# Optimization experiments

Measured on AMD Instinct MI355X. Metric: run time of the kernel, lower is better.

Reference implementation:

```python
import jax, jax.numpy as jnp
import numpy as np

EMBED_DIM = 512
NUM_HEADS = 8
HEAD_DIM = EMBED_DIM // NUM_HEADS
SCALE = HEAD_DIM ** -0.5
B, N = 4, 2048


def setup_inputs() -> dict:
    key = jax.random.key(0)
    ks = jax.random.split(key, 6)
    x = jax.random.normal(ks[0], (B, N, EMBED_DIM), dtype=jnp.float32)
    mask = jnp.ones((B, N, N), dtype=jnp.int32)
    # nn.Linear params: weight [out, in], bias [out]
    lim_qkv = 1.0 / np.sqrt(EMBED_DIM)
    qkv_w = jax.random.uniform(ks[1], (3 * EMBED_DIM, EMBED_DIM), jnp.float32, -lim_qkv, lim_qkv)
    qkv_b = jax.random.uniform(ks[2], (3 * EMBED_DIM,), jnp.float32, -lim_qkv, lim_qkv)
    proj_w = jax.random.uniform(ks[3], (EMBED_DIM, EMBED_DIM), jnp.float32, -lim_qkv, lim_qkv)
    proj_b = jax.random.uniform(ks[4], (EMBED_DIM,), jnp.float32, -lim_qkv, lim_qkv)
    return {"x": x, "qkv_w": qkv_w, "qkv_b": qkv_b, "proj_w": proj_w, "proj_b": proj_b, "mask": mask}


def reference(x, qkv_w, qkv_b, proj_w, proj_b, mask):
    Bb, Nn, C = x.shape
    qkv = (jnp.einsum('bnc,oc->bno', x, qkv_w) + qkv_b).reshape(Bb, Nn, 3, NUM_HEADS, HEAD_DIM)
    qkv = jnp.transpose(qkv, (2, 0, 3, 1, 4))
    q, k, v = qkv[0], qkv[1], qkv[2]
    # full score matrix [B,H,N,N] (faithful to the unfused original)
    attn = jnp.einsum('bhnd,bhmd->bhnm', q, k) * SCALE
    attn = jnp.where(mask[:, None, :, :] == 0, -jnp.inf, attn)
    attn = jax.nn.softmax(attn, axis=-1)
    out = jnp.einsum('bhnm,bhmd->bhnd', attn, v)
    out = jnp.transpose(out, (0, 2, 1, 3)).reshape(Bb, Nn, C)
    out = jnp.einsum('bnc,oc->bno', out, proj_w) + proj_b
    return out
```

## Files before the change

kernel.cpp:

```cpp
#include <hip/hip_runtime.h>
#include <hip/hip_bf16.h>
#include <stdint.h>

#define NB 4
#define NH 8
#define SEQ 2048
#define HD 64
#define CDIM 512

using bf16 = __hip_bfloat16;
typedef __attribute__((ext_vector_type(8))) short short8;
typedef __attribute__((ext_vector_type(4))) short short4_t;
typedef __attribute__((ext_vector_type(4))) float f32x4;

#define NEG_BIG (-3.0e38f)
#define SOFT_C 0.18033688011112042f

__device__ __forceinline__ short bf16_bits(float x) {
  return __builtin_bit_cast(short, __float2bfloat16(x));
}

__device__ __forceinline__ void gld_lds16(const void* g, void* l) {
  __builtin_amdgcn_global_load_lds(
      (const __attribute__((address_space(1))) unsigned int*)g,
      (__attribute__((address_space(3))) unsigned int*)l, 16, 0, 0);
}

#define X4 1048576
#define Q4 196608
#define P4 65536
__global__ __launch_bounds__(256) void prep_cvt(const float* __restrict__ x,
                                                const float* __restrict__ wq,
                                                const float* __restrict__ wp,
                                                short* __restrict__ xb,
                                                short* __restrict__ wqb,
                                                short* __restrict__ wpb) {
  int idx = blockIdx.x * 256 + threadIdx.x;
  int stride = gridDim.x * 256;
  for (int i = idx; i < X4 + Q4 + P4; i += stride) {
    const float* src; short* dst; int off;
    if (i < X4)            { src = x;  dst = xb;  off = i; }
    else if (i < X4 + Q4)  { src = wq; dst = wqb; off = i - X4; }
    else                   { src = wp; dst = wpb; off = i - X4 - Q4; }
    f32x4 v = *(const f32x4*)(src + (size_t)off * 4);
    short4_t o;
    o[0] = bf16_bits(v[0]); o[1] = bf16_bits(v[1]);
    o[2] = bf16_bits(v[2]); o[3] = bf16_bits(v[3]);
    *(short4_t*)(dst + (size_t)off * 4) = o;
  }
}

__global__ __launch_bounds__(256) void qkv_union(const short* __restrict__ Xb,
                                                 const short* __restrict__ Wb,
                                                 const float* __restrict__ bias,
                                                 const int* __restrict__ mask,
                                                 unsigned long long* __restrict__ bits,
                                                 bf16* __restrict__ q,
                                                 bf16* __restrict__ k,
                                                 bf16* __restrict__ vt) {
  __shared__ short Alds[128][32];
  __shared__ short Blds[128][32];
  const int tid = threadIdx.x;
  const int lane = tid & 63;
  const int w = tid >> 6;

  if (blockIdx.x < 512) {
    int wave_g = blockIdx.x * 4 + w;
#pragma unroll 1
    for (int i = 0; i < 32; i++) {
      size_t c = (size_t)i * 2048 + wave_g;
      size_t base = c * 256;
      int v0 = mask[base + 0 * 64 + lane];
      int v1 = mask[base + 1 * 64 + lane];
      int v2 = mask[base + 2 * 64 + lane];
      int v3 = mask[base + 3 * 64 + lane];
      unsigned long long w0 = __ballot(v0 != 0);
      unsigned long long w1 = __ballot(v1 != 0);
      unsigned long long w2 = __ballot(v2 != 0);
      unsigned long long w3 = __ballot(v3 != 0);
      if (lane == 0) {
        bits[c * 4 + 0] = w0; bits[c * 4 + 1] = w1;
        bits[c * 4 + 2] = w2; bits[c * 4 + 3] = w3;
      }
    }
    return;
  }

  const int g = blockIdx.x - 512;
  const int wm = w >> 1, wn = w & 1;
  const int row0 = (g & 63) * 128;
  const int col0 = (g >> 6) * 128;
  const bool isv = (col0 >= 1024);

  f32x4 acc[4][4] = {};
  const int cl = lane & 15;
  const int quad = lane >> 4;

  const int st_r = lane >> 2;
  const int st_gc = (lane & 3) ^ (st_r & 3);
  const int st_col = st_gc * 8;
  const int fc = (quad ^ (cl & 3)) * 8;

  for (int kk = 0; kk < 512; kk += 32) {
#pragma unroll
    for (int t = 0; t < 2; t++) {
      int R = w * 32 + t * 16;
      gld_lds16(&Xb[(size_t)(row0 + R + st_r) * 512 + kk + st_col], &Alds[R][0]);
      gld_lds16(&Wb[(size_t)(col0 + R + st_r) * 512 + kk + st_col], &Blds[R][0]);
    }
    __syncthreads();
    short8 a[4], b[4];
#pragma unroll
    for (int i = 0; i < 4; i++) a[i] = *(const short8*)&Alds[wm * 64 + i * 16 + cl][fc];
#pragma unroll
    for (int j = 0; j < 4; j++) b[j] = *(const short8*)&Blds[wn * 64 + j * 16 + cl][fc];
    if (!isv) {
#pragma unroll
      for (int i = 0; i < 4; i++)
#pragma unroll
        for (int j = 0; j < 4; j++)
          acc[i][j] = __builtin_amdgcn_mfma_f32_16x16x32_bf16(a[i], b[j], acc[i][j], 0, 0, 0);
    } else {
#pragma unroll
      for (int i = 0; i < 4; i++)
#pragma unroll
        for (int j = 0; j < 4; j++)
          acc[i][j] = __builtin_amdgcn_mfma_f32_16x16x32_bf16(b[j], a[i], acc[i][j], 0, 0, 0);
    }
    __syncthreads();
  }

  if (!isv) {
#pragma unroll
    for (int i = 0; i < 4; i++) {
#pragma unroll
      for (int j = 0; j < 4; j++) {
        int col = col0 + wn * 64 + j * 16 + cl;
        float bv = bias[col];
        int which = col >> 9;
        int c = col & 511;
        int h = c >> 6, d = c & 63;
#pragma unroll
        for (int r = 0; r < 4; r++) {
          int row = row0 + wm * 64 + i * 16 + quad * 4 + r;
          int bb = row >> 11, n = row & 2047;
          float val = acc[i][j][r] + bv;
          size_t bh = (size_t)bb * NH + h;
          if (which == 0)      q[(bh * SEQ + n) * HD + d] = __float2bfloat16(val * SOFT_C);
          else                 k[(bh * SEQ + n) * HD + d] = __float2bfloat16(val);
        }
      }
    }
  } else {
#pragma unroll
    for (int i = 0; i < 4; i++) {
#pragma unroll
      for (int j = 0; j < 4; j++) {
        int nrow = row0 + wm * 64 + i * 16 + cl;
        int bb = nrow >> 11, n = nrow & 2047;
#pragma unroll
        for (int r = 0; r < 4; r++) {
          int col = col0 + wn * 64 + j * 16 + quad * 4 + r;
          float bv = bias[col];
          int c = col & 511;
          int h = c >> 6, d = c & 63;
          float val = acc[i][j][r] + bv;
          size_t bh = (size_t)bb * NH + h;
          vt[(bh * HD + d) * SEQ + n] = __float2bfloat16(val);
        }
      }
    }
  }
}

__global__ __launch_bounds__(256) void flash_attn(const bf16* __restrict__ qg,
                                                  const bf16* __restrict__ kg,
                                                  const bf16* __restrict__ vg,
                                                  const unsigned long long* __restrict__ mbits,
                                                  bf16* __restrict__ attn_out) {
  __shared__ short Klds[2][64][64];
  __shared__ short Vlds[2][64][64];
  __shared__ short Plds[4][2][16][72];
  __shared__ unsigned long long Mlds[2][128];

  const int tid = threadIdx.x;
  const int lane = tid & 63;
  const int w = tid >> 6;
  const int qt = blockIdx.x;
  const int h = blockIdx.y;
  const int b = blockIdx.z;

  const size_t bh = (size_t)b * NH + h;
  const bf16* qp = qg + bh * SEQ * HD;
  const bf16* kp = kg + bh * SEQ * HD;
  const bf16* vp = vg + bh * HD * SEQ;

  const int cl = lane & 15;
  const int quad = lane >> 4;
  const int koff = quad * 8;
  const int qrow_w = qt * 128 + w * 32;

  const int c0 = ((quad ^ (cl & 7)) * 8);

  const int st_row = lane >> 3;
  const int st_chunk = (lane & 7) ^ st_row;
  const int st_col = st_chunk * 8;

  short8 aq[2][2];
#pragma unroll
  for (int g = 0; g < 2; g++) {
    aq[g][0] = *(const short8*)&qp[(size_t)(qrow_w + g * 16 + cl) * HD + koff];
    aq[g][1] = *(const short8*)&qp[(size_t)(qrow_w + g * 16 + cl) * HD + 32 + koff];
  }

  f32x4 o[2][4] = {};
  float l_l[2] = {0.f, 0.f};

#pragma unroll
  for (int t = 0; t < 2; t++) {
    int rbase = w * 16 + t * 8;
    gld_lds16(&kp[(size_t)(rbase + st_row) * HD + st_col], &Klds[0][rbase][0]);
    gld_lds16(&vp[(size_t)(rbase + st_row) * SEQ + st_col], &Vlds[0][rbase][0]);
  }
  if (tid < 128) Mlds[0][tid] = mbits[((size_t)b * SEQ + qt * 128 + tid) * (SEQ / 64) + 0];

  for (int kt = 0; kt < 32; kt++) {
    const int cur = kt & 1;
    __syncthreads();

    if (kt + 1 < 32) {
      const int kb2 = (kt + 1) * 64;
#pragma unroll
      for (int t = 0; t < 2; t++) {
        int rbase = w * 16 + t * 8;
        gld_lds16(&kp[(size_t)(kb2 + rbase + st_row) * HD + st_col], &Klds[cur ^ 1][rbase][0]);
        gld_lds16(&vp[(size_t)(rbase + st_row) * SEQ + kb2 + st_col], &Vlds[cur ^ 1][rbase][0]);
      }
      if (tid < 128)
        Mlds[cur ^ 1][tid] = mbits[((size_t)b * SEQ + qt * 128 + tid) * (SEQ / 64) + kt + 1];
    }

    short8 k0[4], k1[4], vb[2][4];
#pragma unroll
    for (int nb = 0; nb < 4; nb++) {
      k0[nb] = *(const short8*)&Klds[cur][nb * 16 + cl][c0];
      k1[nb] = *(const short8*)&Klds[cur][nb * 16 + cl][c0 ^ 32];
    }
#pragma unroll
    for (int ks = 0; ks < 2; ks++)
#pragma unroll
      for (int db = 0; db < 4; db++)
        vb[ks][db] = *(const short8*)&Vlds[cur][db * 16 + cl][c0 ^ (ks * 32)];

    f32x4 s[2][4];
#pragma unroll
    for (int g = 0; g < 2; g++)
#pragma unroll
      for (int nb = 0; nb < 4; nb++) {
        f32x4 z = {0.f, 0.f, 0.f, 0.f};
        z = __builtin_amdgcn_mfma_f32_16x16x32_bf16(k0[nb], aq[g][0], z, 0, 0, 0);
        s[g][nb] = __builtin_amdgcn_mfma_f32_16x16x32_bf16(k1[nb], aq[g][1], z, 0, 0, 0);
      }

#pragma unroll
    for (int g = 0; g < 2; g++) {
      unsigned long long wd = Mlds[cur][w * 32 + g * 16 + cl];
      if (wd != ~0ULL) {
#pragma unroll
        for (int nb = 0; nb < 4; nb++)
#pragma unroll
          for (int r = 0; r < 4; r++)
            if (!((wd >> (nb * 16 + quad * 4 + r)) & 1ULL)) s[g][nb][r] = NEG_BIG;
      }
      float ps = 0.f;
#pragma unroll
      for (int nb = 0; nb < 4; nb++)
#pragma unroll
        for (int r = 0; r < 4; r++) {
          float p = __builtin_amdgcn_exp2f(s[g][nb][r]);
          s[g][nb][r] = p;
          ps += p;
        }
      ps += __shfl_xor(ps, 16);
      ps += __shfl_xor(ps, 32);
      l_l[g] += ps;
#pragma unroll
      for (int nb = 0; nb < 4; nb++) {
        short4_t pk;
        pk[0] = bf16_bits(s[g][nb][0]); pk[1] = bf16_bits(s[g][nb][1]);
        pk[2] = bf16_bits(s[g][nb][2]); pk[3] = bf16_bits(s[g][nb][3]);
        *(short4_t*)&Plds[w][g][cl][nb * 16 + quad * 4] = pk;
      }
    }

#pragma unroll
    for (int g = 0; g < 2; g++)
#pragma unroll
      for (int ks = 0; ks < 2; ks++) {
        short8 pa = *(const short8*)&Plds[w][g][cl][ks * 32 + koff];
#pragma unroll
        for (int db = 0; db < 4; db++)
          o[g][db] = __builtin_amdgcn_mfma_f32_16x16x32_bf16(pa, vb[ks][db], o[g][db], 0, 0, 0);
      }
  }

#pragma unroll
  for (int g = 0; g < 2; g++) {
    float inv = 1.0f / l_l[g];
#pragma unroll
    for (int r = 0; r < 4; r++) {
      float ir = __shfl(inv, (lane & 48) + quad * 4 + r);
      int row = qrow_w + g * 16 + quad * 4 + r;
#pragma unroll
      for (int db = 0; db < 4; db++) {
        float val = o[g][db][r] * ir;
        attn_out[((size_t)b * SEQ + row) * CDIM + h * 64 + db * 16 + cl] = __float2bfloat16(val);
      }
    }
  }
}

__global__ __launch_bounds__(256) void proj_gemm(const bf16* __restrict__ X,
                                                 const short* __restrict__ Wb,
                                                 const float* __restrict__ bias,
                                                 float* __restrict__ out) {
  __shared__ short Alds[128][32];
  __shared__ short Blds[128][32];
  const int tid = threadIdx.x;
  const int lane = tid & 63;
  const int w = tid >> 6;
  const int wm = w >> 1, wn = w & 1;
  const int row0 = blockIdx.x * 128;
  const int col0 = blockIdx.y * 128;

  f32x4 acc[4][4] = {};
  const int cl = lane & 15;
  const int quad = lane >> 4;

  const int st_r = lane >> 2;
  const int st_gc = (lane & 3) ^ (st_r & 3);
  const int st_col = st_gc * 8;
  const int fc = (quad ^ (cl & 3)) * 8;

  for (int kk = 0; kk < 512; kk += 32) {
#pragma unroll
    for (int t = 0; t < 2; t++) {
      int R = w * 32 + t * 16;
      gld_lds16(&X[(size_t)(row0 + R + st_r) * 512 + kk + st_col], &Alds[R][0]);
      gld_lds16(&Wb[(size_t)(col0 + R + st_r) * 512 + kk + st_col], &Blds[R][0]);
    }
    __syncthreads();
    short8 a[4], b[4];
#pragma unroll
    for (int i = 0; i < 4; i++) a[i] = *(const short8*)&Alds[wm * 64 + i * 16 + cl][fc];
#pragma unroll
    for (int j = 0; j < 4; j++) b[j] = *(const short8*)&Blds[wn * 64 + j * 16 + cl][fc];
#pragma unroll
    for (int i = 0; i < 4; i++)
#pragma unroll
      for (int j = 0; j < 4; j++)
        acc[i][j] = __builtin_amdgcn_mfma_f32_16x16x32_bf16(a[i], b[j], acc[i][j], 0, 0, 0);
    __syncthreads();
  }

#pragma unroll
  for (int i = 0; i < 4; i++) {
#pragma unroll
    for (int j = 0; j < 4; j++) {
      int col = col0 + wn * 64 + j * 16 + cl;
      float bv = bias[col];
#pragma unroll
      for (int r = 0; r < 4; r++) {
        int row = row0 + wm * 64 + i * 16 + quad * 4 + r;
        out[(size_t)row * 512 + col] = acc[i][j][r] + bv;
      }
    }
  }
}

extern "C" void kernel_launch(void* const* d_in, const int* in_sizes, int n_in,
                              void* d_out, int out_size, void* d_ws, size_t ws_size,
                              hipStream_t stream) {
  const float* x      = (const float*)d_in[0];
  const float* qkv_w  = (const float*)d_in[1];
  const float* qkv_b  = (const float*)d_in[2];
  const float* proj_w = (const float*)d_in[3];
  const float* proj_b = (const float*)d_in[4];
  const int*   mask   = (const int*)d_in[5];
  float* out = (float*)d_out;

  char* ws = (char*)d_ws;
  bf16* q    = (bf16*)(ws);
  bf16* k    = (bf16*)(ws + 8388608);
  bf16* vt   = (bf16*)(ws + 16777216);
  bf16* attn = (bf16*)(ws + 25165824);
  short* xb  = (short*)(ws + 25165824);
  unsigned long long* mbits = (unsigned long long*)(ws + 33554432);
  short* wqb = (short*)(ws + 35651584);
  short* wpb = (short*)(ws + 37224448);

  prep_cvt<<<dim3(1280), 256, 0, stream>>>(x, qkv_w, proj_w, xb, wqb, wpb);
  qkv_union<<<dim3(512 + 768), 256, 0, stream>>>(xb, wqb, qkv_b, mask, mbits, q, k, vt);
  flash_attn<<<dim3(SEQ / 128, NH, NB), 256, 0, stream>>>(q, k, vt, mbits, attn);
  proj_gemm<<<dim3(64, 4), 256, 0, stream>>>(attn, wpb, proj_b, out);
}
```

Measured before the change: 225.5 us.

## Compute softmax row sums via MFMA with ones, load mask bits into registers

The softmax denominator is now accumulated by an extra MFMA of the bf16 P tile against a ones vector, replacing per-lane sums and cross-lane shuffles. Mask words are prefetched straight from global memory into registers, so the shared-memory mask buffer goes away. K/V fragment reads move ahead of the next-tile prefetch, the barrier moves to the end of the loop, and bf16 packing uses two 32-bit words. This trims VALU and shuffle work but adds MFMA issue per tile, and the row sum now uses bf16-rounded probabilities.

```diff
diff --git a/kernel.cpp b/kernel.cpp
--- a/kernel.cpp
+++ b/kernel.cpp
@@ -11,6 +11,7 @@
 using bf16 = __hip_bfloat16;
 typedef __attribute__((ext_vector_type(8))) short short8;
 typedef __attribute__((ext_vector_type(4))) short short4_t;
+typedef __attribute__((ext_vector_type(2))) unsigned int uint2_t;
 typedef __attribute__((ext_vector_type(4))) float f32x4;
 
 #define NEG_BIG (-3.0e38f)
@@ -18,6 +19,17 @@
 
 __device__ __forceinline__ short bf16_bits(float x) {
   return __builtin_bit_cast(short, __float2bfloat16(x));
+}
+
+__device__ __forceinline__ void pack_p4(float a, float b, float c, float d, short* dst) {
+  unsigned lo = (unsigned)(unsigned short)bf16_bits(a) |
+                ((unsigned)(unsigned short)bf16_bits(b) << 16);
+  unsigned hi = (unsigned)(unsigned short)bf16_bits(c) |
+                ((unsigned)(unsigned short)bf16_bits(d) << 16);
+  uint2_t t;
+  t[0] = lo;
+  t[1] = hi;
+  *(uint2_t*)dst = t;
 }
 
 __device__ __forceinline__ void gld_lds16(const void* g, void* l) {
@@ -181,7 +193,6 @@
   __shared__ short Klds[2][64][64];
   __shared__ short Vlds[2][64][64];
   __shared__ short Plds[4][2][16][72];
-  __shared__ unsigned long long Mlds[2][128];
 
   const int tid = threadIdx.x;
   const int lane = tid & 63;
@@ -206,6 +217,9 @@
   const int st_chunk = (lane & 7) ^ st_row;
   const int st_col = st_chunk * 8;
 
+  const unsigned long long* mr0 = mbits + ((size_t)b * SEQ + qt * 128 + w * 32 + cl) * 32;
+  const unsigned long long* mr1 = mr0 + 16 * 32;
+
   short8 aq[2][2];
 #pragma unroll
   for (int g = 0; g < 2; g++) {
@@ -213,8 +227,12 @@
     aq[g][1] = *(const short8*)&qp[(size_t)(qrow_w + g * 16 + cl) * HD + 32 + koff];
   }
 
+  short8 ones;
+#pragma unroll
+  for (int i = 0; i < 8; i++) ones[i] = (short)0x3F80;
+
   f32x4 o[2][4] = {};
-  float l_l[2] = {0.f, 0.f};
+  f32x4 ol[2] = {};
 
 #pragma unroll
   for (int t = 0; t < 2; t++) {
@@ -222,11 +240,25 @@
     gld_lds16(&kp[(size_t)(rbase + st_row) * HD + st_col], &Klds[0][rbase][0]);
     gld_lds16(&vp[(size_t)(rbase + st_row) * SEQ + st_col], &Vlds[0][rbase][0]);
   }
-  if (tid < 128) Mlds[0][tid] = mbits[((size_t)b * SEQ + qt * 128 + tid) * (SEQ / 64) + 0];
+  unsigned long long wd_next[2];
+  wd_next[0] = mr0[0];
+  wd_next[1] = mr1[0];
+  __syncthreads();
 
   for (int kt = 0; kt < 32; kt++) {
     const int cur = kt & 1;
-    __syncthreads();
+
+    short8 k0[4], k1[4], vb[2][4];
+#pragma unroll
+    for (int nb = 0; nb < 4; nb++) {
+      k0[nb] = *(const short8*)&Klds[cur][nb * 16 + cl][c0];
+      k1[nb] = *(const short8*)&Klds[cur][nb * 16 + cl][c0 ^ 32];
+    }
+#pragma unroll
+    for (int ks = 0; ks < 2; ks++)
+#pragma unroll
+      for (int db = 0; db < 4; db++)
+        vb[ks][db] = *(const short8*)&Vlds[cur][db * 16 + cl][c0 ^ (ks * 32)];
 
     if (kt + 1 < 32) {
       const int kb2 = (kt + 1) * 64;
@@ -236,21 +268,12 @@
         gld_lds16(&kp[(size_t)(kb2 + rbase + st_row) * HD + st_col], &Klds[cur ^ 1][rbase][0]);
         gld_lds16(&vp[(size_t)(rbase + st_row) * SEQ + kb2 + st_col], &Vlds[cur ^ 1][rbase][0]);
       }
-      if (tid < 128)
-        Mlds[cur ^ 1][tid] = mbits[((size_t)b * SEQ + qt * 128 + tid) * (SEQ / 64) + kt + 1];
-    }
-
-    short8 k0[4], k1[4], vb[2][4];
-#pragma unroll
-    for (int nb = 0; nb < 4; nb++) {
-      k0[nb] = *(const short8*)&Klds[cur][nb * 16 + cl][c0];
-      k1[nb] = *(const short8*)&Klds[cur][nb * 16 + cl][c0 ^ 32];
-    }
-#pragma unroll
-    for (int ks = 0; ks < 2; ks++)
-#pragma unroll
-      for (int db = 0; db < 4; db++)
-        vb[ks][db] = *(const short8*)&Vlds[cur][db * 16 + cl][c0 ^ (ks * 32)];
+    }
+    unsigned long long wd[2] = {wd_next[0], wd_next[1]};
+    if (kt + 1 < 32) {
+      wd_next[0] = mr0[kt + 1];
+      wd_next[1] = mr1[kt + 1];
+    }
 
     f32x4 s[2][4];
 #pragma unroll
@@ -264,32 +287,19 @@
 
 #pragma unroll
     for (int g = 0; g < 2; g++) {
-      unsigned long long wd = Mlds[cur][w * 32 + g * 16 + cl];
-      if (wd != ~0ULL) {
+      if (wd[g] != ~0ULL) {
 #pragma unroll
         for (int nb = 0; nb < 4; nb++)
 #pragma unroll
           for (int r = 0; r < 4; r++)
-            if (!((wd >> (nb * 16 + quad * 4 + r)) & 1ULL)) s[g][nb][r] = NEG_BIG;
-      }
-      float ps = 0.f;
-#pragma unroll
-      for (int nb = 0; nb < 4; nb++)
-#pragma unroll
-        for (int r = 0; r < 4; r++) {
-          float p = __builtin_amdgcn_exp2f(s[g][nb][r]);
-          s[g][nb][r] = p;
-          ps += p;
-        }
-      ps += __shfl_xor(ps, 16);
-      ps += __shfl_xor(ps, 32);
-      l_l[g] += ps;
+            if (!((wd[g] >> (nb * 16 + quad * 4 + r)) & 1ULL)) s[g][nb][r] = NEG_BIG;
+      }
 #pragma unroll
       for (int nb = 0; nb < 4; nb++) {
-        short4_t pk;
-        pk[0] = bf16_bits(s[g][nb][0]); pk[1] = bf16_bits(s[g][nb][1]);
-        pk[2] = bf16_bits(s[g][nb][2]); pk[3] = bf16_bits(s[g][nb][3]);
-        *(short4_t*)&Plds[w][g][cl][nb * 16 + quad * 4] = pk;
+#pragma unroll
+        for (int r = 0; r < 4; r++) s[g][nb][r] = __builtin_amdgcn_exp2f(s[g][nb][r]);
+        pack_p4(s[g][nb][0], s[g][nb][1], s[g][nb][2], s[g][nb][3],
+                &Plds[w][g][cl][nb * 16 + quad * 4]);
       }
     }
 
@@ -301,19 +311,21 @@
 #pragma unroll
         for (int db = 0; db < 4; db++)
           o[g][db] = __builtin_amdgcn_mfma_f32_16x16x32_bf16(pa, vb[ks][db], o[g][db], 0, 0, 0);
-      }
+        ol[g] = __builtin_amdgcn_mfma_f32_16x16x32_bf16(pa, ones, ol[g], 0, 0, 0);
+      }
+
+    __syncthreads();
   }
 
 #pragma unroll
   for (int g = 0; g < 2; g++) {
-    float inv = 1.0f / l_l[g];
 #pragma unroll
     for (int r = 0; r < 4; r++) {
-      float ir = __shfl(inv, (lane & 48) + quad * 4 + r);
+      float inv = 1.0f / ol[g][r];
       int row = qrow_w + g * 16 + quad * 4 + r;
 #pragma unroll
       for (int db = 0; db < 4; db++) {
-        float val = o[g][db][r] * ir;
+        float val = o[g][db][r] * inv;
         attn_out[((size_t)b * SEQ + row) * CDIM + h * 64 + db * 16 + cl] = __float2bfloat16(val);
       }
     }
```

After: 222.1 us. No clear change (-1.5%).
